# Optimization experiments

Measured on AMD Instinct MI355X. Metric: run time of the kernel, lower is better.

The kernel has to match this reference:

```python
import jax, jax.numpy as jnp
import numpy as np

B = 8192
DIMS = (512, 768, 1024)
HID = 256
HEADS = 4
HD = HID // HEADS
TOPK = 8


def _layer_norm(x, g, b, eps=1e-5):
    m = x.mean(-1, keepdims=True)
    v = ((x - m) ** 2).mean(-1, keepdims=True)
    return (x - m) / jnp.sqrt(v + eps) * g + b


def setup_inputs() -> dict:
    key = jax.random.key(0)
    ks = jax.random.split(key, 16)
    inp = {}
    for i, d in enumerate(DIMS):
        inp[f"x{i}"] = jax.random.normal(ks[i], (B, d), jnp.float32)
        inp[f"Wp{i}"] = jax.random.normal(ks[3 + i], (d, HID), jnp.float32) / np.float32(np.sqrt(d))
        inp[f"bp{i}"] = jnp.zeros((HID,), jnp.float32)
        inp[f"g{i}"] = jnp.ones((HID,), jnp.float32)
        inp[f"be{i}"] = jnp.zeros((HID,), jnp.float32)
    inp["Win"] = jax.random.normal(ks[10], (HID, 3 * HID), jnp.float32) / np.float32(np.sqrt(HID))
    inp["bin_"] = jnp.zeros((3 * HID,), jnp.float32)
    inp["Wout"] = jax.random.normal(ks[11], (HID, HID), jnp.float32) / np.float32(np.sqrt(HID))
    inp["bout"] = jnp.zeros((HID,), jnp.float32)
    inp["W1"] = jax.random.normal(ks[12], (HID, HID // 2), jnp.float32) / np.float32(np.sqrt(HID))
    inp["b1"] = jnp.zeros((HID // 2,), jnp.float32)
    inp["W2"] = jax.random.normal(ks[13], (HID // 2, 1), jnp.float32) / np.float32(np.sqrt(HID // 2))
    inp["b2"] = jnp.zeros((1,), jnp.float32)
    return inp


def reference(x0, x1, x2, Wp0, bp0, g0, be0, Wp1, bp1, g1, be1, Wp2, bp2, g2, be2,
              Win, bin_, Wout, bout, W1, b1, W2, b2):
    # per-modality projection: Linear -> ReLU -> LayerNorm
    proj = [_layer_norm(jax.nn.relu(x @ Wp + bp), g, b)
            for x, Wp, bp, g, b in ((x0, Wp0, bp0, g0, be0),
                                    (x1, Wp1, bp1, g1, be1),
                                    (x2, Wp2, bp2, g2, be2))]
    seq = jnp.stack(proj, axis=1)  # [B, M=3, HID]
    # torch.nn.MultiheadAttention (batch_first, self-attention)
    qkv = seq @ Win + bin_
    q, k, v = jnp.split(qkv, 3, axis=-1)
    sh = lambda t: t.reshape(B, 3, HEADS, HD).transpose(0, 2, 1, 3)  # [B, H, M, HD]
    q, k, v = sh(q), sh(k), sh(v)
    scores = jnp.einsum('bhsd,bhtd->bhst', q, k) / np.float32(np.sqrt(HD))
    attn = jax.nn.softmax(scores, axis=-1)
    o = jnp.einsum('bhst,bhtd->bhsd', attn, v).transpose(0, 2, 1, 3).reshape(B, 3, HID)
    o = o @ Wout + bout
    fused = o.mean(axis=1)  # [B, HID]
    # row-softmaxed similarity
    sim = jax.nn.softmax(fused @ fused.T, axis=1)  # [B, B]
    vals, idx = jax.lax.top_k(sim, TOPK)  # [B, TOPK]
    # incidence matrix: diag=1 first, then H[neighbor, i] = sim[i, neighbor]
    # (scatter may overwrite the diagonal when i is in its own top-k, as in torch)
    H = jnp.eye(B, dtype=sim.dtype)
    cols = jnp.broadcast_to(jnp.arange(B)[:, None], (B, TOPK))
    H = H.at[idx, cols].set(vals)
    # fallback: empty columns get diagonal 1
    ar = jnp.arange(B)
    colsum = H.sum(axis=0)
    H = H.at[ar, ar].set(jnp.where(colsum == 0.0, 1.0, H[ar, ar]))
    # edge weight predictor: Linear -> ReLU -> Linear -> Sigmoid, clamp
    ew = jax.nn.sigmoid(jax.nn.relu(fused @ W1 + b1) @ W2 + b2)[:, 0]
    ew = jnp.clip(ew, 1e-8)
    return H, ew
```

## Files before the change

kernel.cpp:

```cpp
#include <hip/hip_runtime.h>
#include <hip/hip_bf16.h>
#include <math.h>

#define NB 8192
#define NHID 256

typedef __attribute__((ext_vector_type(8))) short short8;
typedef __attribute__((ext_vector_type(4))) float f32x4;
typedef unsigned short u16;

typedef __attribute__((address_space(3))) unsigned char* as3_u8;
typedef const __attribute__((address_space(1))) unsigned char* as1_cu8;
#define GLOAD_LDS16(g, l) \
    __builtin_amdgcn_global_load_lds((as1_cu8)(g), (as3_u8)(l), 16, 0, 0)

__device__ __forceinline__ void split1(float f, u16& h, u16& l) {
    __hip_bfloat16 hb = __float2bfloat16(f);
    float fh = __bfloat162float(hb);
    __hip_bfloat16 lb = __float2bfloat16(f - fh);
    h = *(u16*)&hb; l = *(u16*)&lb;
}

__global__ __launch_bounds__(256) void wconv_kernel(
    const float* __restrict__ Wp0, const float* __restrict__ Wp1,
    const float* __restrict__ Wp2, const float* __restrict__ Win,
    u16* __restrict__ WTh, u16* __restrict__ WTl,
    u16* __restrict__ WinTh, u16* __restrict__ WinTl)
{
    __shared__ float Ts[32][33];
    const int b = blockIdx.x;
    const int tid = threadIdx.x;
    const float* src; u16 *dh, *dl; int W, outstride, outbase, k0, c0;
    if (b < 576) {
        int base, koff;
        const float* wp;
        if (b < 128)      { base = 0;   koff = 0;    wp = Wp0; }
        else if (b < 320) { base = 128; koff = 512;  wp = Wp1; }
        else              { base = 320; koff = 1280; wp = Wp2; }
        int lb = b - base;
        k0 = (lb >> 3) * 32; c0 = (lb & 7) * 32;
        src = wp; W = 256; dh = WTh; dl = WTl; outstride = 2304; outbase = koff;
    } else {
        int lb = b - 576;
        k0 = (lb & 7) * 32; c0 = (lb >> 3) * 32;
        src = Win; W = 768; dh = WinTh; dl = WinTl; outstride = 256; outbase = 0;
    }
    {
        int r = tid >> 3, cq = (tid & 7) * 4;
        float4 v = *(const float4*)&src[(size_t)(k0 + r) * W + c0 + cq];
        Ts[r][cq] = v.x; Ts[r][cq + 1] = v.y; Ts[r][cq + 2] = v.z; Ts[r][cq + 3] = v.w;
    }
    __syncthreads();
    {
        int c = tid >> 3, r4 = (tid & 7) * 4;
        ushort4 h, l;
        split1(Ts[r4 + 0][c], h.x, l.x);
        split1(Ts[r4 + 1][c], h.y, l.y);
        split1(Ts[r4 + 2][c], h.z, l.z);
        split1(Ts[r4 + 3][c], h.w, l.w);
        size_t off = (size_t)(c0 + c) * outstride + outbase + k0 + r4;
        *(ushort4*)&dh[off] = h;
        *(ushort4*)&dl[off] = l;
    }
}

__global__ __launch_bounds__(256) void proj_mfma_kernel(
    const float* __restrict__ x0, const float* __restrict__ x1, const float* __restrict__ x2,
    const float* __restrict__ bp0, const float* __restrict__ g0, const float* __restrict__ be0,
    const float* __restrict__ bp1, const float* __restrict__ g1, const float* __restrict__ be1,
    const float* __restrict__ bp2, const float* __restrict__ g2, const float* __restrict__ be2,
    const u16* __restrict__ WTh, const u16* __restrict__ WTl,
    u16* __restrict__ seqh, u16* __restrict__ seql)
{
    __shared__ __align__(16) unsigned char smem[51200];

    const int m = blockIdx.y;
    const float* x; const float* bp; const float* g; const float* be; int d, koff;
    if (m == 0)      { x = x0; bp = bp0; g = g0; be = be0; d = 512;  koff = 0; }
    else if (m == 1) { x = x1; bp = bp1; g = g1; be = be1; d = 768;  koff = 512; }
    else             { x = x2; bp = bp2; g = g2; be = be2; d = 1024; koff = 1280; }

    const int tid = threadIdx.x;
    const int lane = tid & 63;
    const int w  = tid >> 6;
    const int lr = lane & 15;
    const int lg = lane >> 4;
    const int r0 = blockIdx.x * 64;

    f32x4 acc[16];
#pragma unroll
    for (int nf = 0; nf < 16; nf++) acc[nf] = (f32x4)0.f;

    const int nkt = d >> 5;
    for (int kt = 0; kt < nkt; kt++) {
        const int k0 = kt << 5;
        __syncthreads();
#pragma unroll
        for (int i = 0; i < 4; i++) {
            int id = i * 256 + tid;
            int col = id >> 2, ks = (id & 3) * 8;
            size_t go = (size_t)col * 2304 + koff + k0 + ks;
            *(short8*)(smem + col * 80 + ks * 2)         = *(const short8*)&WTh[go];
            *(short8*)(smem + 20480 + col * 80 + ks * 2) = *(const short8*)&WTl[go];
        }
#pragma unroll
        for (int i = 0; i < 2; i++) {
            int id = i * 256 + tid;
            int row = id >> 3, kq = (id & 7) * 4;
            float4 v = *(const float4*)&x[(size_t)(r0 + row) * d + k0 + kq];
            ushort4 h, l;
            split1(v.x, h.x, l.x); split1(v.y, h.y, l.y);
            split1(v.z, h.z, l.z); split1(v.w, h.w, l.w);
            *(ushort4*)(smem + 40960 + row * 80 + kq * 2) = h;
            *(ushort4*)(smem + 46080 + row * 80 + kq * 2) = l;
        }
        __syncthreads();

        short8 bvh = *(const short8*)(smem + 40960 + (w * 16 + lr) * 80 + lg * 16);
        short8 bvl = *(const short8*)(smem + 46080 + (w * 16 + lr) * 80 + lg * 16);
#pragma unroll
        for (int nf = 0; nf < 16; nf++) {
            short8 avh = *(const short8*)(smem + (nf * 16 + lr) * 80 + lg * 16);
            short8 avl = *(const short8*)(smem + 20480 + (nf * 16 + lr) * 80 + lg * 16);
            acc[nf] = __builtin_amdgcn_mfma_f32_16x16x32_bf16(avh, bvh, acc[nf], 0, 0, 0);
            acc[nf] = __builtin_amdgcn_mfma_f32_16x16x32_bf16(avl, bvh, acc[nf], 0, 0, 0);
            acc[nf] = __builtin_amdgcn_mfma_f32_16x16x32_bf16(avh, bvl, acc[nf], 0, 0, 0);
        }
    }

    float s = 0.f, s2 = 0.f;
#pragma unroll
    for (int nf = 0; nf < 16; nf++) {
        float4 bpv = *(const float4*)&bp[nf * 16 + lg * 4];
        float bb[4] = {bpv.x, bpv.y, bpv.z, bpv.w};
#pragma unroll
        for (int r = 0; r < 4; r++) {
            float y = fmaxf(acc[nf][r] + bb[r], 0.f);
            acc[nf][r] = y;
            s += y; s2 += y * y;
        }
    }
    s  += __shfl_xor(s, 16);  s  += __shfl_xor(s, 32);
    s2 += __shfl_xor(s2, 16); s2 += __shfl_xor(s2, 32);
    const float meanv = s * (1.f / 256.f);
    const float inv = 1.f / sqrtf(s2 * (1.f / 256.f) - meanv * meanv + 1e-5f);

    const size_t rb = ((size_t)(r0 + w * 16 + lr) * 3 + m) * 256;
#pragma unroll
    for (int nf = 0; nf < 16; nf++) {
        float4 gv  = *(const float4*)&g[nf * 16 + lg * 4];
        float4 bev = *(const float4*)&be[nf * 16 + lg * 4];
        float gc[4] = {gv.x, gv.y, gv.z, gv.w};
        float bc[4] = {bev.x, bev.y, bev.z, bev.w};
        ushort4 h, l;
        float o0 = (acc[nf][0] - meanv) * inv * gc[0] + bc[0];
        float o1 = (acc[nf][1] - meanv) * inv * gc[1] + bc[1];
        float o2 = (acc[nf][2] - meanv) * inv * gc[2] + bc[2];
        float o3 = (acc[nf][3] - meanv) * inv * gc[3] + bc[3];
        split1(o0, h.x, l.x); split1(o1, h.y, l.y);
        split1(o2, h.z, l.z); split1(o3, h.w, l.w);
        *(ushort4*)&seqh[rb + nf * 16 + lg * 4] = h;
        *(ushort4*)&seql[rb + nf * 16 + lg * 4] = l;
    }
}

__global__ __launch_bounds__(256) void qkv_mfma_kernel(
    const u16* __restrict__ seqh, const u16* __restrict__ seql,
    const u16* __restrict__ WinTh, const u16* __restrict__ WinTl,
    const float* __restrict__ bin, float* __restrict__ qkv)
{
    __shared__ __align__(16) unsigned char smem[51200];
    const int tid = threadIdx.x;
    const int lane = tid & 63;
    const int w  = tid >> 6;
    const int lr = lane & 15;
    const int lg = lane >> 4;
    const int c0 = blockIdx.x << 8;
    const int r0 = blockIdx.y << 6;

    f32x4 acc[16];
#pragma unroll
    for (int nf = 0; nf < 16; nf++) acc[nf] = (f32x4)0.f;

    for (int kt = 0; kt < 8; kt++) {
        const int k0 = kt << 5;
        __syncthreads();
#pragma unroll
        for (int i = 0; i < 4; i++) {
            int id = i * 256 + tid;
            int col = id >> 2, ks = (id & 3) * 8;
            size_t go = (size_t)(c0 + col) * 256 + k0 + ks;
            *(short8*)(smem + col * 80 + ks * 2)         = *(const short8*)&WinTh[go];
            *(short8*)(smem + 20480 + col * 80 + ks * 2) = *(const short8*)&WinTl[go];
        }
        {
            int row = tid >> 2, ks = (tid & 3) * 8;
            size_t go = (size_t)(r0 + row) * 256 + k0 + ks;
            *(short8*)(smem + 40960 + row * 80 + ks * 2) = *(const short8*)&seqh[go];
            *(short8*)(smem + 46080 + row * 80 + ks * 2) = *(const short8*)&seql[go];
        }
        __syncthreads();

        short8 bvh = *(const short8*)(smem + 40960 + (w * 16 + lr) * 80 + lg * 16);
        short8 bvl = *(const short8*)(smem + 46080 + (w * 16 + lr) * 80 + lg * 16);
#pragma unroll
        for (int nf = 0; nf < 16; nf++) {
            short8 avh = *(const short8*)(smem + (nf * 16 + lr) * 80 + lg * 16);
            short8 avl = *(const short8*)(smem + 20480 + (nf * 16 + lr) * 80 + lg * 16);
            acc[nf] = __builtin_amdgcn_mfma_f32_16x16x32_bf16(avh, bvh, acc[nf], 0, 0, 0);
            acc[nf] = __builtin_amdgcn_mfma_f32_16x16x32_bf16(avl, bvh, acc[nf], 0, 0, 0);
            acc[nf] = __builtin_amdgcn_mfma_f32_16x16x32_bf16(avh, bvl, acc[nf], 0, 0, 0);
        }
    }

    const size_t rb = (size_t)(r0 + w * 16 + lr) * 768 + c0;
#pragma unroll
    for (int nf = 0; nf < 16; nf++) {
        float4 bv = *(const float4*)&bin[c0 + nf * 16 + lg * 4];
        float4 o = make_float4(acc[nf][0] + bv.x, acc[nf][1] + bv.y,
                               acc[nf][2] + bv.z, acc[nf][3] + bv.w);
        *(float4*)&qkv[rb + nf * 16 + lg * 4] = o;
    }
}

__global__ __launch_bounds__(256) void attn_kernel(
    const float* __restrict__ qkv, const float* __restrict__ Wout,
    const float* __restrict__ bout, const float* __restrict__ W1,
    const float* __restrict__ b1, const float* __restrict__ W2,
    const float* __restrict__ b2, u16* __restrict__ Fh, u16* __restrict__ Fl,
    float* __restrict__ ew)
{
    __shared__ float qk[4][2304];
    __shared__ float at[4][4][3][3];
    __shared__ float ol[12][256];
    __shared__ float fl[4][256];
    __shared__ float h1[4][128];

    const int tid = threadIdx.x;
    const int b0 = blockIdx.x * 4;

#pragma unroll
    for (int i = 0; i < 9; i++) {
        int f4 = i * 256 + tid;
        int lb = f4 / 576, rem = f4 - lb * 576;
        *(float4*)&qk[lb][rem * 4] =
            *(const float4*)&qkv[(size_t)(b0 + lb) * 2304 + rem * 4];
    }
    __syncthreads();

    if (tid < 144) {
        int lb = tid / 36, r = tid % 36;
        int h = r / 9, s = (r / 3) % 3, t = r % 3;
        const float* qp = &qk[lb][s * 768 + h * 64];
        const float* kp = &qk[lb][t * 768 + 256 + h * 64];
        float sum = 0.f;
#pragma unroll
        for (int dd = 0; dd < 64; dd++) sum = fmaf(qp[dd], kp[dd], sum);
        at[lb][h][s][t] = sum * 0.125f;
    }
    __syncthreads();

    if (tid < 48) {
        int lb = tid / 12, h = (tid / 3) % 4, s = tid % 3;
        float v0 = at[lb][h][s][0], v1 = at[lb][h][s][1], v2 = at[lb][h][s][2];
        float mx = fmaxf(v0, fmaxf(v1, v2));
        float e0 = expf(v0 - mx), e1 = expf(v1 - mx), e2 = expf(v2 - mx);
        float inv = 1.f / (e0 + e1 + e2);
        at[lb][h][s][0] = e0 * inv; at[lb][h][s][1] = e1 * inv; at[lb][h][s][2] = e2 * inv;
    }
    __syncthreads();

    {
        int j = tid, h = j >> 6;
#pragma unroll
        for (int lb = 0; lb < 4; lb++)
#pragma unroll
            for (int s = 0; s < 3; s++) {
                float o = at[lb][h][s][0] * qk[lb][0 * 768 + 512 + j]
                        + at[lb][h][s][1] * qk[lb][1 * 768 + 512 + j]
                        + at[lb][h][s][2] * qk[lb][2 * 768 + 512 + j];
                ol[lb * 3 + s][j] = o;
            }
    }
    __syncthreads();

    {
        const int txx = tid & 63, lbb = tid >> 6;
        float a0[4] = {0, 0, 0, 0}, a1[4] = {0, 0, 0, 0}, a2[4] = {0, 0, 0, 0};
        for (int k = 0; k < 256; k++) {
            float4 w = *(const float4*)&Wout[(size_t)k * 256 + txx * 4];
            float wv[4] = {w.x, w.y, w.z, w.w};
            float o0 = ol[lbb * 3 + 0][k], o1 = ol[lbb * 3 + 1][k], o2 = ol[lbb * 3 + 2][k];
#pragma unroll
            for (int c = 0; c < 4; c++) {
                a0[c] = fmaf(o0, wv[c], a0[c]);
                a1[c] = fmaf(o1, wv[c], a1[c]);
                a2[c] = fmaf(o2, wv[c], a2[c]);
            }
        }
        float4 bo = *(const float4*)&bout[txx * 4];
        float bc[4] = {bo.x, bo.y, bo.z, bo.w};
        float f[4];
        u16 hq[4], lq[4];
#pragma unroll
        for (int c = 0; c < 4; c++) {
            f[c] = ((a0[c] + bc[c]) + (a1[c] + bc[c]) + (a2[c] + bc[c])) * (1.f / 3.f);
            split1(f[c], hq[c], lq[c]);
        }
        *(float4*)&fl[lbb][txx * 4] = make_float4(f[0], f[1], f[2], f[3]);
        uint2 hp, lp;
        hp.x = (unsigned)hq[0] | ((unsigned)hq[1] << 16);
        hp.y = (unsigned)hq[2] | ((unsigned)hq[3] << 16);
        lp.x = (unsigned)lq[0] | ((unsigned)lq[1] << 16);
        lp.y = (unsigned)lq[2] | ((unsigned)lq[3] << 16);
        *(uint2*)&Fh[(size_t)(b0 + lbb) * NHID + txx * 4] = hp;
        *(uint2*)&Fl[(size_t)(b0 + lbb) * NHID + txx * 4] = lp;
    }
    __syncthreads();

    {
        int lb = tid >> 6, j = tid & 63;
        float s0 = 0.f, s1 = 0.f;
        for (int k = 0; k < 256; k++) {
            float fv = fl[lb][k];
            s0 = fmaf(fv, W1[(size_t)k * 128 + j], s0);
            s1 = fmaf(fv, W1[(size_t)k * 128 + j + 64], s1);
        }
        h1[lb][j]      = fmaxf(s0 + b1[j], 0.f);
        h1[lb][j + 64] = fmaxf(s1 + b1[j + 64], 0.f);
    }
    __syncthreads();
    if (tid < 4) {
        float s = 0.f;
        for (int j = 0; j < 128; j++) s = fmaf(h1[tid][j], W2[j], s);
        s += b2[0];
        float e = 1.f / (1.f + expf(-s));
        ew[b0 + tid] = fmaxf(e, 1e-8f);
    }
}

__global__ __launch_bounds__(256) void sim_mfma_kernel(
    const u16* __restrict__ Fh, const u16* __restrict__ Fl, float* __restrict__ C)
{
    __shared__ __align__(16) unsigned char smem[32768];

    const int tid  = threadIdx.x;
    const int lane = tid & 63;
    const int w    = tid >> 6;
    const int wr   = w >> 1;
    const int wc   = w & 1;
    const int lr   = lane & 15;
    const int lg   = lane >> 4;

    const int orig = blockIdx.x;
    const int wg   = ((orig & 7) << 9) | (orig >> 3);
    const int i0   = (wg >> 6) << 7;
    const int j0   = (wg & 63) << 7;

    const int srow  = lane >> 3;
    const int sslot = (lane & 7) ^ srow;
    const int acol  = sslot * 8;

    f32x4 acc[4][4];
#pragma unroll
    for (int a = 0; a < 4; a++)
#pragma unroll
        for (int b = 0; b < 4; b++) acc[a][b] = (f32x4)0.f;

    for (int kt = 0; kt < 12; kt++) {
        const int seg  = kt >> 2;
        const int kloc = (kt & 3) << 6;
        const u16* Ag = (seg == 1) ? Fl : Fh;
        const u16* Bg = (seg == 2) ? Fl : Fh;

        __syncthreads();
#pragma unroll
        for (int i = 0; i < 4; i++) {
            const int rbase = w * 32 + i * 8;
            GLOAD_LDS16(&Ag[(size_t)(i0 + rbase + srow) * NHID + kloc + acol],
                        smem + rbase * 128);
            GLOAD_LDS16(&Bg[(size_t)(j0 + rbase + srow) * NHID + kloc + acol],
                        smem + 16384 + rbase * 128);
        }
        __syncthreads();

#pragma unroll
        for (int ks = 0; ks < 2; ks++) {
            short8 av[4], bv[4];
            const int slotx = ((ks * 4 + lg) ^ (lr & 7)) * 16;
#pragma unroll
            for (int f = 0; f < 4; f++) {
                av[f] = *(const short8*)(smem + (wr * 64 + f * 16 + lr) * 128 + slotx);
                bv[f] = *(const short8*)(smem + 16384 + (wc * 64 + f * 16 + lr) * 128 + slotx);
            }
#pragma unroll
            for (int fj = 0; fj < 4; fj++)
#pragma unroll
                for (int fi = 0; fi < 4; fi++)
                    acc[fj][fi] = __builtin_amdgcn_mfma_f32_16x16x32_bf16(
                        bv[fj], av[fi], acc[fj][fi], 0, 0, 0);
        }
    }

#pragma unroll
    for (int fj = 0; fj < 4; fj++)
#pragma unroll
        for (int fi = 0; fi < 4; fi++) {
            const int r = i0 + wr * 64 + fi * 16 + lr;
            const int c = j0 + wc * 64 + fj * 16 + lg * 4;
            *(f32x4*)&C[(size_t)r * NB + c] = acc[fj][fi];
        }
}

__global__ __launch_bounds__(256) void topk_kernel(
    float* __restrict__ logits, float* __restrict__ topv, int* __restrict__ topi)
{
    __shared__ float wv[8][4];
    __shared__ int   sidx[8];
    __shared__ float red[4];
    const int row = blockIdx.x;
    const int tid = threadIdx.x;
    float* L = &logits[(size_t)row * NB];

    if (tid < 8) sidx[tid] = 0x7fffffff;

    float v[32];
#pragma unroll
    for (int q = 0; q < 8; q++) {
        float4 x4 = *(const float4*)&L[(q * 256 + tid) * 4];
        v[q * 4 + 0] = x4.x; v[q * 4 + 1] = x4.y;
        v[q * 4 + 2] = x4.z; v[q * 4 + 3] = x4.w;
    }
    float g[8];
#pragma unroll
    for (int q = 0; q < 8; q++)
        g[q] = fmaxf(fmaxf(v[q * 4], v[q * 4 + 1]), fmaxf(v[q * 4 + 2], v[q * 4 + 3]));

    __syncthreads();

    float rank_v[8]; int rank_i[8];
#pragma unroll
    for (int r = 0; r < 8; r++) {
        float t = fmaxf(fmaxf(fmaxf(g[0], g[1]), fmaxf(g[2], g[3])),
                        fmaxf(fmaxf(g[4], g[5]), fmaxf(g[6], g[7])));
        float wm = t;
#pragma unroll
        for (int off = 1; off < 64; off <<= 1)
            wm = fmaxf(wm, __shfl_xor(wm, off));
        if ((tid & 63) == 0) wv[r][tid >> 6] = wm;
        __syncthreads();
        const float m = fmaxf(fmaxf(wv[r][0], wv[r][1]), fmaxf(wv[r][2], wv[r][3]));
        if (t == m) {
            int best = 0x7fffffff;
#pragma unroll
            for (int q = 0; q < 8; q++)
#pragma unroll
                for (int c = 0; c < 4; c++)
                    if (v[q * 4 + c] == m) {
                        int gi = (q * 256 + tid) * 4 + c;
                        best = min(best, gi);
                    }
            atomicMin(&sidx[r], best);
        }
        __syncthreads();
        const int idx = sidx[r];
        rank_v[r] = m; rank_i[r] = idx;
        if (((idx >> 2) & 255) == tid) {
            const int q = idx >> 10;
#pragma unroll
            for (int qq = 0; qq < 8; qq++) if (qq == q) {
                const int c = idx & 3;
#pragma unroll
                for (int cc = 0; cc < 4; cc++) if (cc == c)
                    v[qq * 4 + cc] = -INFINITY;
                g[qq] = fmaxf(fmaxf(v[qq * 4], v[qq * 4 + 1]),
                              fmaxf(v[qq * 4 + 2], v[qq * 4 + 3]));
            }
        }
    }

    const float mx = rank_v[0];
    float ps = 0.f;
#pragma unroll
    for (int q = 0; q < 32; q++) ps += __expf(v[q] - mx);
#pragma unroll
    for (int off = 1; off < 64; off <<= 1) ps += __shfl_xor(ps, off);
    if ((tid & 63) == 0) red[tid >> 6] = ps;
    __syncthreads();
    if (tid == 0) {
        float er[8];
        float esum = 0.f;
#pragma unroll
        for (int r = 0; r < 8; r++) { er[r] = __expf(rank_v[r] - mx); esum += er[r]; }
        const float inv = 1.f / (red[0] + red[1] + red[2] + red[3] + esum);
#pragma unroll
        for (int r = 0; r < 8; r++) {
            topv[(size_t)row * 8 + r] = er[r] * inv;
            topi[(size_t)row * 8 + r] = rank_i[r];
        }
    }

    __syncthreads();
#pragma unroll
    for (int q = 0; q < 8; q++) {
        int c4 = (q * 256 + tid) * 4;
        float4 o;
        o.x = (c4 == row)     ? 1.f : 0.f;
        o.y = (c4 + 1 == row) ? 1.f : 0.f;
        o.z = (c4 + 2 == row) ? 1.f : 0.f;
        o.w = (c4 + 3 == row) ? 1.f : 0.f;
        *(float4*)&L[c4] = o;
    }
}

__global__ __launch_bounds__(256) void scatter_kernel(
    const float* __restrict__ topv, const int* __restrict__ topi, float* __restrict__ H)
{
    int t = blockIdx.x * 256 + threadIdx.x;
    int i = t >> 3;
    H[(size_t)topi[t] * NB + i] = topv[t];
}

extern "C" void kernel_launch(void* const* d_in, const int* in_sizes, int n_in,
                              void* d_out, int out_size, void* d_ws, size_t ws_size,
                              hipStream_t stream)
{
    const float* x0  = (const float*)d_in[0];
    const float* Wp0 = (const float*)d_in[1];
    const float* bp0 = (const float*)d_in[2];
    const float* g0  = (const float*)d_in[3];
    const float* be0 = (const float*)d_in[4];
    const float* x1  = (const float*)d_in[5];
    const float* Wp1 = (const float*)d_in[6];
    const float* bp1 = (const float*)d_in[7];
    const float* g1  = (const float*)d_in[8];
    const float* be1 = (const float*)d_in[9];
    const float* x2  = (const float*)d_in[10];
    const float* Wp2 = (const float*)d_in[11];
    const float* bp2 = (const float*)d_in[12];
    const float* g2  = (const float*)d_in[13];
    const float* be2 = (const float*)d_in[14];
    const float* Win = (const float*)d_in[15];
    const float* bin = (const float*)d_in[16];
    const float* Wout= (const float*)d_in[17];
    const float* bout= (const float*)d_in[18];
    const float* W1  = (const float*)d_in[19];
    const float* b1  = (const float*)d_in[20];
    const float* W2  = (const float*)d_in[21];
    const float* b2  = (const float*)d_in[22];

    float* out = (float*)d_out;
    char*  outc = (char*)d_out;

    float* qkv   = out;
    u16*   seqh  = (u16*)(outc + 75497472);
    u16*   seql  = (u16*)(outc + 88080384);
    u16*   WTh   = (u16*)(outc + 100663296);
    u16*   WTl   = (u16*)(outc + 101842944);
    u16*   WinTh = (u16*)(outc + 103022592);
    u16*   WinTl = (u16*)(outc + 103415808);
    u16*   Fh   = (u16*)d_ws;
    u16*   Fl   = (u16*)((char*)d_ws + (4u << 20));
    float* topv = (float*)((char*)d_ws + (8u << 20));
    int*   topi = (int*)((char*)d_ws + (8u << 20) + 262144);
    float* ew   = out + (size_t)NB * NB;

    wconv_kernel<<<768, 256, 0, stream>>>(Wp0, Wp1, Wp2, Win, WTh, WTl, WinTh, WinTl);
    proj_mfma_kernel<<<dim3(128, 3), 256, 0, stream>>>(
        x0, x1, x2, bp0, g0, be0, bp1, g1, be1, bp2, g2, be2, WTh, WTl, seqh, seql);
    qkv_mfma_kernel<<<dim3(3, 384), 256, 0, stream>>>(seqh, seql, WinTh, WinTl, bin, qkv);
    attn_kernel<<<2048, 256, 0, stream>>>(qkv, Wout, bout, W1, b1, W2, b2, Fh, Fl, ew);
    sim_mfma_kernel<<<4096, 256, 0, stream>>>(Fh, Fl, out);
    topk_kernel<<<8192, 256, 0, stream>>>(out, topv, topi);
    scatter_kernel<<<256, 256, 0, stream>>>(topv, topi, out);
}
```

Before: 824.9 us.

## Fuse similarity GEMM with online softmax and top-k, split rows across eight column chunks

Replaces the sim GEMM that wrote the full 8192x8192 logits matrix, and the top-k kernel that read it back, with a fused kernel. The fused kernel computes 128x64 tiles into LDS and keeps a per-thread online softmax max/sum and a running top-8 with index tie-breaking, over eight column splits per row block. A small merge kernel combines the partial results, and a separate nontemporal fill kernel writes the identity matrix. This removes a 256MB write and read of logits but runs only 512 blocks, with serial per-element insertion-sort work and redundant A-tile reloads per column tile.

```diff
diff --git a/kernel.cpp b/kernel.cpp
--- a/kernel.cpp
+++ b/kernel.cpp
@@ -19,6 +19,23 @@
     float fh = __bfloat162float(hb);
     __hip_bfloat16 lb = __float2bfloat16(f - fh);
     h = *(u16*)&hb; l = *(u16*)&lb;
+}
+
+__device__ __forceinline__ bool better(float a, int ia, float b, int ib) {
+    return (a > b) || (a == b && ia < ib);
+}
+
+__device__ __forceinline__ void ins8(float v, int ix, float (&tv)[8], int (&ti)[8]) {
+    if (better(v, ix, tv[7], ti[7])) {
+        tv[7] = v; ti[7] = ix;
+#pragma unroll
+        for (int s = 7; s > 0; s--) {
+            if (better(tv[s], ti[s], tv[s - 1], ti[s - 1])) {
+                float tf = tv[s]; tv[s] = tv[s - 1]; tv[s - 1] = tf;
+                int   tt = ti[s]; ti[s] = ti[s - 1]; ti[s - 1] = tt;
+            }
+        }
+    }
 }
 
 __global__ __launch_bounds__(256) void wconv_kernel(
@@ -339,177 +356,173 @@
     }
 }
 
-__global__ __launch_bounds__(256) void sim_mfma_kernel(
-    const u16* __restrict__ Fh, const u16* __restrict__ Fl, float* __restrict__ C)
-{
-    __shared__ __align__(16) unsigned char smem[32768];
+__global__ __launch_bounds__(256) void fused_sim_topk_kernel(
+    const u16* __restrict__ Fh, const u16* __restrict__ Fl,
+    float* __restrict__ Ml, float* __restrict__ Vsp, int* __restrict__ Isp)
+{
+    __shared__ __align__(16) unsigned char smem[59392];
+    float* Cs = (float*)(smem + 24576);
 
     const int tid  = threadIdx.x;
     const int lane = tid & 63;
     const int w    = tid >> 6;
-    const int wr   = w >> 1;
-    const int wc   = w & 1;
     const int lr   = lane & 15;
     const int lg   = lane >> 4;
-
-    const int orig = blockIdx.x;
-    const int wg   = ((orig & 7) << 9) | (orig >> 3);
-    const int i0   = (wg >> 6) << 7;
-    const int j0   = (wg & 63) << 7;
-
-    const int srow  = lane >> 3;
-    const int sslot = (lane & 7) ^ srow;
-    const int acol  = sslot * 8;
-
-    f32x4 acc[4][4];
-#pragma unroll
-    for (int a = 0; a < 4; a++)
-#pragma unroll
-        for (int b = 0; b < 4; b++) acc[a][b] = (f32x4)0.f;
-
-    for (int kt = 0; kt < 12; kt++) {
-        const int seg  = kt >> 2;
-        const int kloc = (kt & 3) << 6;
-        const u16* Ag = (seg == 1) ? Fl : Fh;
-        const u16* Bg = (seg == 2) ? Fl : Fh;
-
+    const int rowblk = blockIdx.x >> 3;
+    const int split  = blockIdx.x & 7;
+    const int i0 = rowblk << 7;
+    const int j0 = split << 10;
+
+    const int srow = lane >> 3;
+    const int acol = ((lane & 7) ^ srow) * 8;
+
+    const int mrow = tid >> 1;
+    const int mhalf = tid & 1;
+
+    float tv[8]; int ti[8];
+#pragma unroll
+    for (int s = 0; s < 8; s++) { tv[s] = -INFINITY; ti[s] = 0x7fffffff; }
+    float rm = -INFINITY, rl = 0.f;
+
+    for (int t = 0; t < 16; t++) {
+        const int jt = j0 + (t << 6);
+        f32x4 acc[4][2];
+#pragma unroll
+        for (int a = 0; a < 4; a++)
+#pragma unroll
+            for (int b = 0; b < 2; b++) acc[a][b] = (f32x4)0.f;
+
+        for (int kt = 0; kt < 12; kt++) {
+            const int seg  = kt >> 2;
+            const int kloc = (kt & 3) << 6;
+            const u16* Ag = (seg == 1) ? Fl : Fh;
+            const u16* Bg = (seg == 2) ? Fl : Fh;
+
+            __syncthreads();
+#pragma unroll
+            for (int i = 0; i < 4; i++) {
+                const int rbase = w * 32 + i * 8;
+                GLOAD_LDS16(&Ag[(size_t)(i0 + rbase + srow) * NHID + kloc + acol],
+                            smem + rbase * 128);
+            }
+#pragma unroll
+            for (int i = 0; i < 2; i++) {
+                const int rbase = (w + i * 4) * 8;
+                GLOAD_LDS16(&Bg[(size_t)(jt + rbase + srow) * NHID + kloc + acol],
+                            smem + 16384 + rbase * 128);
+            }
+            __syncthreads();
+
+#pragma unroll
+            for (int ks = 0; ks < 2; ks++) {
+                const int slotx = ((ks * 4 + lg) ^ (lr & 7)) * 16;
+                short8 av[2], bv[4];
+#pragma unroll
+                for (int fi = 0; fi < 2; fi++)
+                    av[fi] = *(const short8*)(smem + (w * 32 + fi * 16 + lr) * 128 + slotx);
+#pragma unroll
+                for (int fj = 0; fj < 4; fj++)
+                    bv[fj] = *(const short8*)(smem + 16384 + (fj * 16 + lr) * 128 + slotx);
+#pragma unroll
+                for (int fj = 0; fj < 4; fj++)
+#pragma unroll
+                    for (int fi = 0; fi < 2; fi++)
+                        acc[fj][fi] = __builtin_amdgcn_mfma_f32_16x16x32_bf16(
+                            bv[fj], av[fi], acc[fj][fi], 0, 0, 0);
+            }
+        }
+
+#pragma unroll
+        for (int fj = 0; fj < 4; fj++)
+#pragma unroll
+            for (int fi = 0; fi < 2; fi++)
+                *(f32x4*)&Cs[(w * 32 + fi * 16 + lr) * 68 + fj * 16 + lg * 4] = acc[fj][fi];
         __syncthreads();
-#pragma unroll
-        for (int i = 0; i < 4; i++) {
-            const int rbase = w * 32 + i * 8;
-            GLOAD_LDS16(&Ag[(size_t)(i0 + rbase + srow) * NHID + kloc + acol],
-                        smem + rbase * 128);
-            GLOAD_LDS16(&Bg[(size_t)(j0 + rbase + srow) * NHID + kloc + acol],
-                        smem + 16384 + rbase * 128);
-        }
-        __syncthreads();
-
-#pragma unroll
-        for (int ks = 0; ks < 2; ks++) {
-            short8 av[4], bv[4];
-            const int slotx = ((ks * 4 + lg) ^ (lr & 7)) * 16;
-#pragma unroll
-            for (int f = 0; f < 4; f++) {
-                av[f] = *(const short8*)(smem + (wr * 64 + f * 16 + lr) * 128 + slotx);
-                bv[f] = *(const short8*)(smem + 16384 + (wc * 64 + f * 16 + lr) * 128 + slotx);
-            }
-#pragma unroll
-            for (int fj = 0; fj < 4; fj++)
-#pragma unroll
-                for (int fi = 0; fi < 4; fi++)
-                    acc[fj][fi] = __builtin_amdgcn_mfma_f32_16x16x32_bf16(
-                        bv[fj], av[fi], acc[fj][fi], 0, 0, 0);
-        }
-    }
-
-#pragma unroll
-    for (int fj = 0; fj < 4; fj++)
-#pragma unroll
-        for (int fi = 0; fi < 4; fi++) {
-            const int r = i0 + wr * 64 + fi * 16 + lr;
-            const int c = j0 + wc * 64 + fj * 16 + lg * 4;
-            *(f32x4*)&C[(size_t)r * NB + c] = acc[fj][fi];
-        }
-}
-
-__global__ __launch_bounds__(256) void topk_kernel(
-    float* __restrict__ logits, float* __restrict__ topv, int* __restrict__ topi)
-{
-    __shared__ float wv[8][4];
-    __shared__ int   sidx[8];
-    __shared__ float red[4];
-    const int row = blockIdx.x;
-    const int tid = threadIdx.x;
-    float* L = &logits[(size_t)row * NB];
-
-    if (tid < 8) sidx[tid] = 0x7fffffff;
-
-    float v[32];
-#pragma unroll
-    for (int q = 0; q < 8; q++) {
-        float4 x4 = *(const float4*)&L[(q * 256 + tid) * 4];
-        v[q * 4 + 0] = x4.x; v[q * 4 + 1] = x4.y;
-        v[q * 4 + 2] = x4.z; v[q * 4 + 3] = x4.w;
-    }
-    float g[8];
-#pragma unroll
-    for (int q = 0; q < 8; q++)
-        g[q] = fmaxf(fmaxf(v[q * 4], v[q * 4 + 1]), fmaxf(v[q * 4 + 2], v[q * 4 + 3]));
-
-    __syncthreads();
-
-    float rank_v[8]; int rank_i[8];
-#pragma unroll
-    for (int r = 0; r < 8; r++) {
-        float t = fmaxf(fmaxf(fmaxf(g[0], g[1]), fmaxf(g[2], g[3])),
-                        fmaxf(fmaxf(g[4], g[5]), fmaxf(g[6], g[7])));
-        float wm = t;
-#pragma unroll
-        for (int off = 1; off < 64; off <<= 1)
-            wm = fmaxf(wm, __shfl_xor(wm, off));
-        if ((tid & 63) == 0) wv[r][tid >> 6] = wm;
-        __syncthreads();
-        const float m = fmaxf(fmaxf(wv[r][0], wv[r][1]), fmaxf(wv[r][2], wv[r][3]));
-        if (t == m) {
-            int best = 0x7fffffff;
-#pragma unroll
-            for (int q = 0; q < 8; q++)
-#pragma unroll
-                for (int c = 0; c < 4; c++)
-                    if (v[q * 4 + c] == m) {
-                        int gi = (q * 256 + tid) * 4 + c;
-                        best = min(best, gi);
-                    }
-            atomicMin(&sidx[r], best);
-        }
-        __syncthreads();
-        const int idx = sidx[r];
-        rank_v[r] = m; rank_i[r] = idx;
-        if (((idx >> 2) & 255) == tid) {
-            const int q = idx >> 10;
-#pragma unroll
-            for (int qq = 0; qq < 8; qq++) if (qq == q) {
-                const int c = idx & 3;
-#pragma unroll
-                for (int cc = 0; cc < 4; cc++) if (cc == c)
-                    v[qq * 4 + cc] = -INFINITY;
-                g[qq] = fmaxf(fmaxf(v[qq * 4], v[qq * 4 + 1]),
-                              fmaxf(v[qq * 4 + 2], v[qq * 4 + 3]));
-            }
-        }
-    }
-
-    const float mx = rank_v[0];
-    float ps = 0.f;
-#pragma unroll
-    for (int q = 0; q < 32; q++) ps += __expf(v[q] - mx);
-#pragma unroll
-    for (int off = 1; off < 64; off <<= 1) ps += __shfl_xor(ps, off);
-    if ((tid & 63) == 0) red[tid >> 6] = ps;
-    __syncthreads();
-    if (tid == 0) {
-        float er[8];
-        float esum = 0.f;
-#pragma unroll
-        for (int r = 0; r < 8; r++) { er[r] = __expf(rank_v[r] - mx); esum += er[r]; }
-        const float inv = 1.f / (red[0] + red[1] + red[2] + red[3] + esum);
-#pragma unroll
-        for (int r = 0; r < 8; r++) {
-            topv[(size_t)row * 8 + r] = er[r] * inv;
-            topi[(size_t)row * 8 + r] = rank_i[r];
-        }
-    }
-
-    __syncthreads();
-#pragma unroll
-    for (int q = 0; q < 8; q++) {
-        int c4 = (q * 256 + tid) * 4;
-        float4 o;
-        o.x = (c4 == row)     ? 1.f : 0.f;
-        o.y = (c4 + 1 == row) ? 1.f : 0.f;
-        o.z = (c4 + 2 == row) ? 1.f : 0.f;
-        o.w = (c4 + 3 == row) ? 1.f : 0.f;
-        *(float4*)&L[c4] = o;
+
+#pragma unroll
+        for (int q = 0; q < 8; q++) {
+            f32x4 c4 = *(const f32x4*)&Cs[mrow * 68 + mhalf * 32 + q * 4];
+            const int gbase = jt + mhalf * 32 + q * 4;
+#pragma unroll
+            for (int e = 0; e < 4; e++) {
+                float val = c4[e];
+                int gi = gbase + e;
+                if (val > rm) { rl = rl * __expf(rm - val) + 1.f; rm = val; }
+                else          { rl += __expf(val - rm); }
+                ins8(val, gi, tv, ti);
+            }
+        }
+    }
+
+    float pm = __shfl_xor(rm, 1);
+    float pl = __shfl_xor(rl, 1);
+    float M2 = fmaxf(rm, pm);
+    float L2 = rl * __expf(rm - M2) + pl * __expf(pm - M2);
+#pragma unroll
+    for (int s = 0; s < 8; s++) {
+        float pv = __shfl_xor(tv[s], 1);
+        int   pi = __shfl_xor(ti[s], 1);
+        if (mhalf == 0) ins8(pv, pi, tv, ti);
+    }
+    if (mhalf == 0) {
+        const int rec = ((i0 + mrow) << 3) + split;
+        Ml[rec * 2]     = M2;
+        Ml[rec * 2 + 1] = L2;
+#pragma unroll
+        for (int s = 0; s < 8; s++) {
+            Vsp[rec * 8 + s] = tv[s];
+            Isp[rec * 8 + s] = ti[s];
+        }
+    }
+}
+
+__global__ __launch_bounds__(64) void merge_topk_kernel(
+    const float* __restrict__ Ml, const float* __restrict__ Vsp,
+    const int* __restrict__ Isp, float* __restrict__ topv, int* __restrict__ topi)
+{
+    const int row = blockIdx.x * 64 + threadIdx.x;
+    const int rb = row * 8;
+
+    float M = -INFINITY;
+#pragma unroll
+    for (int s = 0; s < 8; s++) M = fmaxf(M, Ml[(rb + s) * 2]);
+    float L = 0.f;
+#pragma unroll
+    for (int s = 0; s < 8; s++)
+        L += Ml[(rb + s) * 2 + 1] * __expf(Ml[(rb + s) * 2] - M);
+
+    float tv[8]; int ti[8];
+#pragma unroll
+    for (int s = 0; s < 8; s++) { tv[s] = -INFINITY; ti[s] = 0x7fffffff; }
+#pragma unroll
+    for (int s = 0; s < 8; s++)
+#pragma unroll
+        for (int k = 0; k < 8; k++)
+            ins8(Vsp[(rb + s) * 8 + k], Isp[(rb + s) * 8 + k], tv, ti);
+
+    const float invL = 1.f / L;
+#pragma unroll
+    for (int k = 0; k < 8; k++) {
+        topv[rb + k] = __expf(tv[k] - M) * invL;
+        topi[rb + k] = ti[k];
+    }
+}
+
+__global__ __launch_bounds__(256) void hfill_kernel(float* __restrict__ H)
+{
+    size_t base = (size_t)blockIdx.x * 256 + threadIdx.x;
+#pragma unroll
+    for (int i = 0; i < 8; i++) {
+        size_t id = base + (size_t)i * 2097152;
+        size_t p = id * 4;
+        int r = (int)(p >> 13);
+        int c = (int)(p & 8191);
+        f32x4 o;
+        o[0] = (c == r)     ? 1.f : 0.f;
+        o[1] = (c + 1 == r) ? 1.f : 0.f;
+        o[2] = (c + 2 == r) ? 1.f : 0.f;
+        o[3] = (c + 3 == r) ? 1.f : 0.f;
+        __builtin_nontemporal_store(o, (f32x4*)&H[p]);
     }
 }
 
@@ -559,6 +572,9 @@
     u16*   WTl   = (u16*)(outc + 101842944);
     u16*   WinTh = (u16*)(outc + 103022592);
     u16*   WinTl = (u16*)(outc + 103415808);
+    float* Ml    = (float*)(outc + 104857600);
+    float* Vsp   = (float*)(outc + 105906176);
+    int*   Isp   = (int*)(outc + 108003328);
     u16*   Fh   = (u16*)d_ws;
     u16*   Fl   = (u16*)((char*)d_ws + (4u << 20));
     float* topv = (float*)((char*)d_ws + (8u << 20));
@@ -570,7 +586,8 @@
         x0, x1, x2, bp0, g0, be0, bp1, g1, be1, bp2, g2, be2, WTh, WTl, seqh, seql);
     qkv_mfma_kernel<<<dim3(3, 384), 256, 0, stream>>>(seqh, seql, WinTh, WinTl, bin, qkv);
     attn_kernel<<<2048, 256, 0, stream>>>(qkv, Wout, bout, W1, b1, W2, b2, Fh, Fl, ew);
-    sim_mfma_kernel<<<4096, 256, 0, stream>>>(Fh, Fl, out);
-    topk_kernel<<<8192, 256, 0, stream>>>(out, topv, topi);
+    fused_sim_topk_kernel<<<512, 256, 0, stream>>>(Fh, Fl, Ml, Vsp, Isp);
+    merge_topk_kernel<<<128, 64, 0, stream>>>(Ml, Vsp, Isp, topv, topi);
+    hfill_kernel<<<8192, 256, 0, stream>>>(out);
     scatter_kernel<<<256, 256, 0, stream>>>(topv, topi, out);
 }
```

New measurement: 1.597 ms. 1.94x slower.
